# Performance work log

Measured on AMD Instinct MI355X. Metric: run time of the kernel, lower is better.

## Reference

```python
import jax, jax.numpy as jnp
import numpy as np

BN_EPS = 1e-3  # TF batch_norm default epsilon


def _three_nn(xyz1, xyz2):
    # xyz1: [B,N,3], xyz2: [B,M,3] -> squared dists [B,N,3], idx [B,N,3]
    d = (jnp.sum(xyz1 * xyz1, -1)[:, :, None]
         - 2.0 * jnp.einsum('bnd,bmd->bnm', xyz1, xyz2)
         + jnp.sum(xyz2 * xyz2, -1)[:, None, :])  # [B,N,M]
    neg, idx = jax.lax.top_k(-d, 3)
    return -neg, idx


def _conv_bn(x, W, b, g, beta, act):
    # 1x1 conv == dense over channel dim; BN over batch+point axes (B,N)
    y = jnp.einsum('bnc,cd->bnd', x, W) + b
    mu = jnp.mean(y, axis=(0, 1))
    var = jnp.var(y, axis=(0, 1))
    y = (y - mu) * jax.lax.rsqrt(var + BN_EPS) * g + beta
    return jax.nn.relu(y) if act else y


def setup_inputs() -> dict:
    key = jax.random.key(0)
    ks = jax.random.split(key, 6)
    B, N, M, C1, C2 = 16, 4096, 1024, 128, 256
    xyz1 = jax.random.normal(ks[0], (B, N, 3), jnp.float32)
    xyz2 = jax.random.normal(ks[1], (B, M, 3), jnp.float32)
    points1 = jax.random.normal(ks[2], (B, N, C1), jnp.float32)
    points2 = jax.random.normal(ks[3], (B, M, C2), jnp.float32)
    Cin = C1 + C2
    W0 = jax.random.normal(ks[4], (Cin, 256), jnp.float32) * (1.0 / np.sqrt(Cin))
    W1 = jax.random.normal(ks[5], (256, 128), jnp.float32) * (1.0 / np.sqrt(256))
    return {
        'xyz1': xyz1, 'points1': points1, 'xyz2': xyz2, 'points2': points2,
        'W0': W0, 'b0': jnp.zeros((256,), jnp.float32),
        'g0': jnp.ones((256,), jnp.float32), 'be0': jnp.zeros((256,), jnp.float32),
        'W1': W1, 'b1': jnp.zeros((128,), jnp.float32),
        'g1': jnp.ones((128,), jnp.float32), 'be1': jnp.zeros((128,), jnp.float32),
    }


def reference(xyz1, points1, xyz2, points2, W0, b0, g0, be0, W1, b1, g1, be1):
    dist, idx = _three_nn(xyz1, xyz2)            # [B,N,3]
    dist = jnp.maximum(dist, 1e-10)
    w = 1.0 / dist
    w = w / jnp.sum(w, axis=2, keepdims=True)    # [B,N,3]
    B = points2.shape[0]
    bidx = jnp.arange(B)[:, None, None]
    nbr = points2[bidx, idx]                     # [B,N,3,C2] gather
    interp = jnp.einsum('bnk,bnkc->bnc', w, nbr)
    x = jnp.concatenate([interp, points1], axis=2)  # [B,N,C1+C2]
    x = _conv_bn(x, W0, b0, g0, be0, act=True)
    x = _conv_bn(x, W1, b1, g1, be1, act=True)   # last_mlp_activation=True
    return x
```

## Files before the change

kernel.cpp:

```cpp
#include <hip/hip_runtime.h>
#include <hip/hip_bf16.h>
#include <stdint.h>

typedef __attribute__((ext_vector_type(4))) float f32x4;
typedef __attribute__((ext_vector_type(2))) float f32x2;
typedef __attribute__((ext_vector_type(8))) __bf16 bf16x8;

__device__ __forceinline__ unsigned short f2bf(float f) {
  unsigned u = __float_as_uint(f);
  unsigned r = (u + 0x7fffu + ((u >> 16) & 1u)) >> 16;
  return (unsigned short)r;
}
__device__ __forceinline__ float bf2f(unsigned short h) {
  return __uint_as_float(((unsigned)h) << 16);
}

__device__ __forceinline__ void load_lds16(const void* g, void* l) {
  __builtin_amdgcn_global_load_lds(
      (const __attribute__((address_space(1))) unsigned int*)g,
      (__attribute__((address_space(3))) unsigned int*)l, 16, 0, 0);
}

__device__ __forceinline__ void vwait(int n) {
  switch (n) {
    case 8: asm volatile("s_waitcnt vmcnt(8)" ::: "memory"); break;
    case 6: asm volatile("s_waitcnt vmcnt(6)" ::: "memory"); break;
    case 4: asm volatile("s_waitcnt vmcnt(4)" ::: "memory"); break;
    case 3: asm volatile("s_waitcnt vmcnt(3)" ::: "memory"); break;
    default: asm volatile("s_waitcnt vmcnt(0)" ::: "memory"); break;
  }
  __builtin_amdgcn_sched_barrier(0);
}

__global__ __launch_bounds__(256) void prep_kernel(
    const float* __restrict__ W0, const float* __restrict__ W1,
    const float* __restrict__ P2f, unsigned short* __restrict__ W0t,
    unsigned short* __restrict__ W1t, unsigned short* __restrict__ P2) {
  int id = blockIdx.x * 256 + threadIdx.x;
  if (id < 256 * 384) {
    int n = id / 384, k = id - n * 384;
    W0t[id] = f2bf(W0[k * 256 + n]);
  }
  if (id < 128 * 256) {
    int n = id / 256, k = id - n * 256;
    W1t[id] = f2bf(W1[k * 128 + n]);
  }
  if (id < 1048576) {
    f32x4 v = ((const f32x4*)P2f)[id];
    ushort4 o = make_ushort4(f2bf(v[0]), f2bf(v[1]), f2bf(v[2]), f2bf(v[3]));
    ((ushort4*)P2)[id] = o;
  }
}

__global__ __launch_bounds__(256) void three_nn_kernel(
    const float* __restrict__ xyz1, const float* __restrict__ xyz2,
    float* __restrict__ W3, int* __restrict__ I3) {
  __shared__ __align__(16) float sx[1024];
  __shared__ __align__(16) float sy[1024];
  __shared__ __align__(16) float sz[1024];
  __shared__ __align__(16) float sn[1024];
  const int b = blockIdx.y;
  const int n0 = blockIdx.x * 32;
  const int tid = threadIdx.x;

  const float* xb = xyz2 + (size_t)b * 3072;
  for (int i = tid; i < 1024; i += 256) {
    float x = xb[i * 3 + 0], y = xb[i * 3 + 1], z = xb[i * 3 + 2];
    sx[i] = x; sy[i] = y; sz[i] = z;
    sn[i] = x * x + y * y + z * z;
  }
  __syncthreads();

  const int pt = tid >> 3, q = tid & 7;
  const int n = n0 + pt;
  const float* p = xyz1 + ((size_t)b * 4096 + n) * 3;
  const float px = p[0], py = p[1], pz = p[2];
  const float cx = -2.f * px, cy = -2.f * py, cz = -2.f * pz;

  float d0 = 3e38f, d1 = 3e38f, d2 = 3e38f;
  int i0 = 0, i1 = 0, i2 = 0;
  auto ins = [&](float e, int j) {
    const bool c0 = e < d0, c1 = e < d1, c2 = e < d2;
    const float nd2 = c1 ? d1 : (c2 ? e : d2);
    const int   ni2 = c1 ? i1 : (c2 ? j : i2);
    const float nd1 = c0 ? d0 : (c1 ? e : d1);
    const int   ni1 = c0 ? i0 : (c1 ? j : i1);
    d0 = c0 ? e : d0; i0 = c0 ? j : i0;
    d1 = nd1; i1 = ni1;
    d2 = nd2; i2 = ni2;
  };

  const f32x4* vx = (const f32x4*)sx;
  const f32x4* vy = (const f32x4*)sy;
  const f32x4* vz = (const f32x4*)sz;
  const f32x4* vn = (const f32x4*)sn;
  for (int jj = 0; jj < 32; jj++) {
    const int c = jj * 8 + q;
    f32x4 ax = vx[c], ay = vy[c], az = vz[c], an = vn[c];
#pragma unroll
    for (int u = 0; u < 4; u++) {
      float d = fmaf(ax[u], cx, fmaf(ay[u], cy, fmaf(az[u], cz, an[u])));
      ins(d, c * 4 + u);
    }
  }
#pragma unroll
  for (int off = 1; off <= 4; off <<= 1) {
    float e0 = __shfl_xor(d0, off, 64);
    float e1 = __shfl_xor(d1, off, 64);
    float e2 = __shfl_xor(d2, off, 64);
    int j0 = __shfl_xor(i0, off, 64);
    int j1 = __shfl_xor(i1, off, 64);
    int j2 = __shfl_xor(i2, off, 64);
    ins(e0, j0); ins(e1, j1); ins(e2, j2);
  }

  if (q == 0) {
    const float pn = fmaf(px, px, fmaf(py, py, pz * pz));
    float t0 = fmaxf(d0 + pn, 1e-10f);
    float t1 = fmaxf(d1 + pn, 1e-10f);
    float t2 = fmaxf(d2 + pn, 1e-10f);
    float w0 = 1.f / t0, w1 = 1.f / t1, w2 = 1.f / t2;
    float inv = 1.f / (w0 + w1 + w2);
    const int row = b * 4096 + n;
    W3[row * 3 + 0] = w0 * inv;
    W3[row * 3 + 1] = w1 * inv;
    W3[row * 3 + 2] = w2 * inv;
    I3[row * 3 + 0] = (b << 10) + i0;
    I3[row * 3 + 1] = (b << 10) + i1;
    I3[row * 3 + 2] = (b << 10) + i2;
  }
}

__global__ __launch_bounds__(256) void interp_concat_kernel(
    const float* __restrict__ points1, const unsigned short* __restrict__ P2,
    const float* __restrict__ W3, const int* __restrict__ I3,
    unsigned short* __restrict__ X) {
  const int gw = blockIdx.x * 4 + (threadIdx.x >> 6);
  const int lane = threadIdx.x & 63;
#pragma unroll 2
  for (int pp = 0; pp < 8; pp++) {
    const int row = gw * 8 + pp;
    const float w0 = W3[row * 3 + 0], w1 = W3[row * 3 + 1], w2 = W3[row * 3 + 2];
    const int g0 = I3[row * 3 + 0], g1 = I3[row * 3 + 1], g2 = I3[row * 3 + 2];
    const ushort4 a0 = *(const ushort4*)(P2 + (size_t)g0 * 256 + lane * 4);
    const ushort4 a1 = *(const ushort4*)(P2 + (size_t)g1 * 256 + lane * 4);
    const ushort4 a2 = *(const ushort4*)(P2 + (size_t)g2 * 256 + lane * 4);
    float o0 = bf2f(a0.x) * w0 + bf2f(a1.x) * w1 + bf2f(a2.x) * w2;
    float o1 = bf2f(a0.y) * w0 + bf2f(a1.y) * w1 + bf2f(a2.y) * w2;
    float o2 = bf2f(a0.z) * w0 + bf2f(a1.z) * w1 + bf2f(a2.z) * w2;
    float o3 = bf2f(a0.w) * w0 + bf2f(a1.w) * w1 + bf2f(a2.w) * w2;
    unsigned int lo = (unsigned)f2bf(o0) | ((unsigned)f2bf(o1) << 16);
    unsigned int hi = (unsigned)f2bf(o2) | ((unsigned)f2bf(o3) << 16);
    *(uint2*)(X + (size_t)row * 384 + lane * 4) = make_uint2(lo, hi);
    const f32x2 qv = ((const f32x2*)(points1 + (size_t)row * 128))[lane];
    unsigned int pq = (unsigned)f2bf(qv.x) | ((unsigned)f2bf(qv.y) << 16);
    *(unsigned int*)(X + (size_t)row * 384 + 256 + lane * 2) = pq;
  }
}

__global__ __launch_bounds__(512) void gemm1_kernel(
    const unsigned short* __restrict__ A, const unsigned short* __restrict__ Bt,
    const float* __restrict__ bvec, unsigned short* __restrict__ Y,
    float* __restrict__ ssum, float* __restrict__ ssq) {
  __shared__ __align__(16) char smem[131072];
  unsigned short* S = (unsigned short*)smem;
  const int m0 = blockIdx.x * 256;
  const int tid = threadIdx.x;
  const int wv = tid >> 6, lane = tid & 63;
  const int wm = wv >> 2, wn = wv & 3;
  f32x4 acc[8][4] = {};

  auto stage = [&](int t) {
    const int k0 = t * 32;
    unsigned short* Ab = S + (t & 3) * 16384;
    unsigned short* Bb = Ab + 8192;
#pragma unroll
    for (int i = 0; i < 2; i++) {
      const int c = (wv * 2 + i) * 64 + lane;
      const int row = c >> 2, kp = c & 3;
      const int gk = (kp ^ (row & 3)) * 8;
      load_lds16(A + (size_t)(m0 + row) * 384 + k0 + gk, Ab + (wv * 2 + i) * 512);
      load_lds16(Bt + (size_t)row * 384 + k0 + gk, Bb + (wv * 2 + i) * 512);
    }
  };

  stage(0); stage(1); stage(2);
  for (int t = 0; t < 12; ++t) {
    const int w = 11 - t;
    vwait(w >= 2 ? 8 : w * 4);
    __builtin_amdgcn_s_barrier();
    __builtin_amdgcn_sched_barrier(0);
    if (t < 9) stage(t + 3);
    const unsigned short* Ab = S + (t & 3) * 16384;
    const unsigned short* Bb = Ab + 8192;
    const int q = lane >> 4;
    bf16x8 af[8], bfr[4];
#pragma unroll
    for (int mf = 0; mf < 8; mf++) {
      const int r = wm * 128 + mf * 16 + (lane & 15);
      af[mf] = *(const bf16x8*)(Ab + r * 32 + (q ^ (r & 3)) * 8);
    }
#pragma unroll
    for (int nf = 0; nf < 4; nf++) {
      const int c = wn * 64 + nf * 16 + (lane & 15);
      bfr[nf] = *(const bf16x8*)(Bb + c * 32 + (q ^ (c & 3)) * 8);
    }
    __builtin_amdgcn_s_setprio(1);
#pragma unroll
    for (int mf = 0; mf < 8; mf++)
#pragma unroll
      for (int nf = 0; nf < 4; nf++)
        acc[mf][nf] = __builtin_amdgcn_mfma_f32_16x16x32_bf16(
            af[mf], bfr[nf], acc[mf][nf], 0, 0, 0);
    __builtin_amdgcn_s_setprio(0);
  }
  __syncthreads();

  float s[4] = {0, 0, 0, 0}, s2[4] = {0, 0, 0, 0};
  unsigned short* ep = S + wv * 8192;
#pragma unroll
  for (int mf = 0; mf < 8; mf++) {
#pragma unroll
    for (int nf = 0; nf < 4; nf++) {
      const float bv = bvec[wn * 64 + nf * 16 + (lane & 15)];
      f32x4 v = acc[mf][nf];
#pragma unroll
      for (int r = 0; r < 4; r++) {
        float y = v[r] + bv;
        s[nf] += y;
        s2[nf] += y * y;
        ep[(mf * 16 + (lane >> 4) * 4 + r) * 64 + nf * 16 + (lane & 15)] =
            f2bf(y);
      }
    }
  }
#pragma unroll
  for (int it = 0; it < 16; it++) {
    const int rr = it * 8 + (lane >> 3);
    *(uint4*)(Y + (size_t)(m0 + wm * 128 + rr) * 256 + wn * 64 + (lane & 7) * 8) =
        *(const uint4*)(ep + rr * 64 + (lane & 7) * 8);
  }

#pragma unroll
  for (int nf = 0; nf < 4; nf++) {
    s[nf] += __shfl_xor(s[nf], 16, 64);
    s[nf] += __shfl_xor(s[nf], 32, 64);
    s2[nf] += __shfl_xor(s2[nf], 16, 64);
    s2[nf] += __shfl_xor(s2[nf], 32, 64);
  }
  if (lane < 16) {
#pragma unroll
    for (int nf = 0; nf < 4; nf++) {
      const int col = wn * 64 + nf * 16 + lane;
      atomicAdd(&ssum[col], s[nf]);
      atomicAdd(&ssq[col], s2[nf]);
    }
  }
}

__device__ __forceinline__ uint4 bnpack8(bf16x8 r, f32x4 s0, f32x4 s1,
                                         f32x4 c0, f32x4 c1) {
  unsigned short o[8];
#pragma unroll
  for (int j = 0; j < 8; j++) {
    const float sj = j < 4 ? s0[j] : s1[j - 4];
    const float cj = j < 4 ? c0[j] : c1[j - 4];
    o[j] = f2bf(fmaxf(0.f, fmaf((float)r[j], sj, cj)));
  }
  return make_uint4((unsigned)o[0] | ((unsigned)o[1] << 16),
                    (unsigned)o[2] | ((unsigned)o[3] << 16),
                    (unsigned)o[4] | ((unsigned)o[5] << 16),
                    (unsigned)o[6] | ((unsigned)o[7] << 16));
}

__global__ __launch_bounds__(512) void gemm2_kernel(
    const unsigned short* __restrict__ Yin, const unsigned short* __restrict__ Bt,
    const float* __restrict__ scale1, const float* __restrict__ bias1,
    const float* __restrict__ bvec, unsigned short* __restrict__ Y2,
    float* __restrict__ ssum, float* __restrict__ ssq) {
  __shared__ __align__(16) char smem[100352];
  unsigned short* S = (unsigned short*)smem;
  float* scL = (float*)(smem + 98304);
  float* biL = scL + 256;
  const int m0 = blockIdx.x * 256;
  const int tid = threadIdx.x;
  const int wv = tid >> 6, lane = tid & 63;
  const int wm = wv >> 2, wn = wv & 3;
  f32x4 acc[8][2] = {};

  if (tid < 256) scL[tid] = scale1[tid];
  else biL[tid - 256] = bias1[tid - 256];
  __syncthreads();

  bf16x8 arg[3][2];
  auto stageT = [&](int t, bf16x8(&ar)[2]) {
    const int k0 = t * 32;
#pragma unroll
    for (int j = 0; j < 2; j++) {
      const int c = tid + j * 512;
      const int row = c >> 2, kp = c & 3;
      const int gk = (kp ^ (row & 3)) * 8;
      ar[j] = *(const bf16x8*)(Yin + (size_t)(m0 + row) * 256 + k0 + gk);
    }
    const int cb = wv * 64 + lane;
    const int rowb = cb >> 2, kpb = cb & 3;
    const int gkb = (kpb ^ (rowb & 3)) * 8;
    load_lds16(Bt + (size_t)rowb * 256 + k0 + gkb,
               S + (t & 3) * 12288 + 8192 + wv * 512);
  };

  stageT(0, arg[0]); stageT(1, arg[1]); stageT(2, arg[2]);
#pragma unroll
  for (int t = 0; t < 8; ++t) {
    const int w = 7 - t;
    vwait(w >= 2 ? 6 : w * 3);
    unsigned short* Ab = S + (t & 3) * 12288;
#pragma unroll
    for (int j = 0; j < 2; j++) {
      const int c = tid + j * 512;
      const int row = c >> 2, kp = c & 3;
      const int gk = (kp ^ (row & 3)) * 8;
      const int kch = t * 32 + gk;
      const f32x4 sA = *(const f32x4*)(scL + kch);
      const f32x4 sB = *(const f32x4*)(scL + kch + 4);
      const f32x4 cA = *(const f32x4*)(biL + kch);
      const f32x4 cB = *(const f32x4*)(biL + kch + 4);
      *(uint4*)(Ab + c * 8) = bnpack8(arg[t % 3][j], sA, sB, cA, cB);
    }
    asm volatile("s_waitcnt lgkmcnt(0)" ::: "memory");
    __builtin_amdgcn_sched_barrier(0);
    __builtin_amdgcn_s_barrier();
    __builtin_amdgcn_sched_barrier(0);
    if (t < 5) stageT(t + 3, arg[t % 3]);
    const unsigned short* Bb = S + (t & 3) * 12288 + 8192;
    const int q = lane >> 4;
    bf16x8 af[8], bfr[2];
#pragma unroll
    for (int mf = 0; mf < 8; mf++) {
      const int r = wm * 128 + mf * 16 + (lane & 15);
      af[mf] = *(const bf16x8*)(Ab + r * 32 + (q ^ (r & 3)) * 8);
    }
#pragma unroll
    for (int nf = 0; nf < 2; nf++) {
      const int c = wn * 32 + nf * 16 + (lane & 15);
      bfr[nf] = *(const bf16x8*)(Bb + c * 32 + (q ^ (c & 3)) * 8);
    }
    __builtin_amdgcn_s_setprio(1);
#pragma unroll
    for (int mf = 0; mf < 8; mf++)
#pragma unroll
      for (int nf = 0; nf < 2; nf++)
        acc[mf][nf] = __builtin_amdgcn_mfma_f32_16x16x32_bf16(
            af[mf], bfr[nf], acc[mf][nf], 0, 0, 0);
    __builtin_amdgcn_s_setprio(0);
  }
  __syncthreads();

  float s[2] = {0, 0}, s2[2] = {0, 0};
  unsigned short* ep = S + wv * 4096;
#pragma unroll
  for (int mf = 0; mf < 8; mf++) {
#pragma unroll
    for (int nf = 0; nf < 2; nf++) {
      const float bv = bvec[wn * 32 + nf * 16 + (lane & 15)];
      f32x4 v = acc[mf][nf];
#pragma unroll
      for (int r = 0; r < 4; r++) {
        float y = v[r] + bv;
        s[nf] += y;
        s2[nf] += y * y;
        ep[(mf * 16 + (lane >> 4) * 4 + r) * 32 + nf * 16 + (lane & 15)] =
            f2bf(y);
      }
    }
  }
#pragma unroll
  for (int it = 0; it < 8; it++) {
    const int rr = it * 16 + (lane >> 2);
    *(uint4*)(Y2 + (size_t)(m0 + wm * 128 + rr) * 128 + wn * 32 + (lane & 3) * 8) =
        *(const uint4*)(ep + rr * 32 + (lane & 3) * 8);
  }

#pragma unroll
  for (int nf = 0; nf < 2; nf++) {
    s[nf] += __shfl_xor(s[nf], 16, 64);
    s[nf] += __shfl_xor(s[nf], 32, 64);
    s2[nf] += __shfl_xor(s2[nf], 16, 64);
    s2[nf] += __shfl_xor(s2[nf], 32, 64);
  }
  if (lane < 16) {
#pragma unroll
    for (int nf = 0; nf < 2; nf++) {
      const int col = wn * 32 + nf * 16 + lane;
      atomicAdd(&ssum[col], s[nf]);
      atomicAdd(&ssq[col], s2[nf]);
    }
  }
}

__global__ void bn_fin_kernel(const float* __restrict__ ssum,
                              const float* __restrict__ ssq,
                              const float* __restrict__ g,
                              const float* __restrict__ be,
                              float* __restrict__ scale,
                              float* __restrict__ bias, int C) {
  int c = blockIdx.x * blockDim.x + threadIdx.x;
  if (c < C) {
    const float invN = 1.0f / 65536.0f;
    float mu = ssum[c] * invN;
    float var = ssq[c] * invN - mu * mu;
    float sc = g[c] * rsqrtf(var + 1e-3f);
    scale[c] = sc;
    bias[c] = be[c] - mu * sc;
  }
}

__global__ __launch_bounds__(256) void bnrelu_out_kernel(
    const unsigned short* __restrict__ Y2, const float* __restrict__ scale,
    const float* __restrict__ bias, float* __restrict__ out) {
  const size_t i = ((size_t)blockIdx.x * 256 + threadIdx.x) * 8;
  const int c0 = (int)(i & 127);
  uint4 v = *(const uint4*)(Y2 + i);
  const f32x4 sA = *(const f32x4*)(scale + c0);
  const f32x4 sB = *(const f32x4*)(scale + c0 + 4);
  const f32x4 bA = *(const f32x4*)(bias + c0);
  const f32x4 bB = *(const f32x4*)(bias + c0 + 4);
  unsigned int w[4] = {v.x, v.y, v.z, v.w};
  f32x4 o0, o1;
#pragma unroll
  for (int q = 0; q < 2; q++) {
    o0[q * 2 + 0] = fmaxf(0.f, fmaf(bf2f((unsigned short)(w[q] & 0xffff)), sA[q * 2 + 0], bA[q * 2 + 0]));
    o0[q * 2 + 1] = fmaxf(0.f, fmaf(bf2f((unsigned short)(w[q] >> 16)),   sA[q * 2 + 1], bA[q * 2 + 1]));
    o1[q * 2 + 0] = fmaxf(0.f, fmaf(bf2f((unsigned short)(w[q + 2] & 0xffff)), sB[q * 2 + 0], bB[q * 2 + 0]));
    o1[q * 2 + 1] = fmaxf(0.f, fmaf(bf2f((unsigned short)(w[q + 2] >> 16)),   sB[q * 2 + 1], bB[q * 2 + 1]));
  }
  *(f32x4*)(out + i) = o0;
  *(f32x4*)(out + i + 4) = o1;
}

extern "C" void kernel_launch(void* const* d_in, const int* in_sizes, int n_in,
                              void* d_out, int out_size, void* d_ws,
                              size_t ws_size, hipStream_t stream) {
  const float* xyz1 = (const float*)d_in[0];
  const float* points1 = (const float*)d_in[1];
  const float* xyz2 = (const float*)d_in[2];
  const float* points2 = (const float*)d_in[3];
  const float* W0 = (const float*)d_in[4];
  const float* b0 = (const float*)d_in[5];
  const float* g0 = (const float*)d_in[6];
  const float* be0 = (const float*)d_in[7];
  const float* W1 = (const float*)d_in[8];
  const float* b1 = (const float*)d_in[9];
  const float* g1 = (const float*)d_in[10];
  const float* be1 = (const float*)d_in[11];

  char* ws = (char*)d_ws;
  unsigned short* X = (unsigned short*)(ws);
  unsigned short* Y2 = (unsigned short*)(ws);
  unsigned short* Y = (unsigned short*)(ws + 50331648);
  unsigned short* P2 = (unsigned short*)(ws + 50331648);
  float* W3 = (float*)(ws + 50331648 + 8388608);
  int* I3 = (int*)(ws + 50331648 + 8388608 + 786432);
  unsigned short* W0t = (unsigned short*)(ws + 83886080);
  unsigned short* W1t = (unsigned short*)(ws + 84082688);
  float* stats = (float*)(ws + 84148224);
  float* sum1 = stats, *sq1 = stats + 256, *scale1 = stats + 512, *bias1 = stats + 768;
  float* sum2 = stats + 1024, *sq2 = stats + 1152, *scale2 = stats + 1280, *bias2 = stats + 1408;
  float* outF = (float*)d_out;

  hipMemsetAsync(stats, 0, 1536 * sizeof(float), stream);
  prep_kernel<<<4096, 256, 0, stream>>>(W0, W1, points2, W0t, W1t, P2);
  three_nn_kernel<<<dim3(128, 16), 256, 0, stream>>>(xyz1, xyz2, W3, I3);
  interp_concat_kernel<<<2048, 256, 0, stream>>>(points1, P2, W3, I3, X);
  gemm1_kernel<<<256, 512, 0, stream>>>(X, W0t, b0, Y, sum1, sq1);
  bn_fin_kernel<<<1, 256, 0, stream>>>(sum1, sq1, g0, be0, scale1, bias1, 256);
  gemm2_kernel<<<256, 512, 0, stream>>>(Y, W1t, scale1, bias1, b1, Y2, sum2, sq2);
  bn_fin_kernel<<<1, 128, 0, stream>>>(sum2, sq2, g1, be1, scale2, bias2, 128);
  bnrelu_out_kernel<<<4096, 256, 0, stream>>>(Y2, scale2, bias2, outF);
}
```

Before: 139.2 us.

## Fuse BatchNorm finalize and apply into GEMMs via cooperative grid sync

Both GEMM kernels now keep their accumulators in registers, atomically reduce the per-channel statistics, grid-synchronize, compute the BN scale and bias locally, then apply BN+ReLU before writing. Y now holds the post-ReLU activations and gemm2 writes the final fp32 output directly. This removes the two bn_fin launches, the separate bnrelu_out pass, the bf16 Y2 round trip and the on-the-fly BN in gemm2's A-staging, which now uses plain direct-to-LDS loads. In exchange it depends on cooperative launch with all 256 blocks co-resident and adds a grid-wide barrier stall per GEMM.

```diff
diff --git a/kernel.cpp b/kernel.cpp
--- a/kernel.cpp
+++ b/kernel.cpp
@@ -1,6 +1,9 @@
 #include <hip/hip_runtime.h>
 #include <hip/hip_bf16.h>
+#include <hip/hip_cooperative_groups.h>
 #include <stdint.h>
+
+namespace cg = cooperative_groups;
 
 typedef __attribute__((ext_vector_type(4))) float f32x4;
 typedef __attribute__((ext_vector_type(2))) float f32x2;
@@ -160,7 +163,8 @@
 
 __global__ __launch_bounds__(512) void gemm1_kernel(
     const unsigned short* __restrict__ A, const unsigned short* __restrict__ Bt,
-    const float* __restrict__ bvec, unsigned short* __restrict__ Y,
+    const float* __restrict__ bvec, const float* __restrict__ g0,
+    const float* __restrict__ be0, unsigned short* __restrict__ Y,
     float* __restrict__ ssum, float* __restrict__ ssq) {
   __shared__ __align__(16) char smem[131072];
   unsigned short* S = (unsigned short*)smem;
@@ -214,33 +218,22 @@
             af[mf], bfr[nf], acc[mf][nf], 0, 0, 0);
     __builtin_amdgcn_s_setprio(0);
   }
-  __syncthreads();
-
-  float s[4] = {0, 0, 0, 0}, s2[4] = {0, 0, 0, 0};
-  unsigned short* ep = S + wv * 8192;
-#pragma unroll
-  for (int mf = 0; mf < 8; mf++) {
+
+  float bvl[4], s[4] = {0, 0, 0, 0}, s2[4] = {0, 0, 0, 0};
+#pragma unroll
+  for (int nf = 0; nf < 4; nf++) bvl[nf] = bvec[wn * 64 + nf * 16 + (lane & 15)];
+#pragma unroll
+  for (int mf = 0; mf < 8; mf++)
 #pragma unroll
     for (int nf = 0; nf < 4; nf++) {
-      const float bv = bvec[wn * 64 + nf * 16 + (lane & 15)];
       f32x4 v = acc[mf][nf];
 #pragma unroll
       for (int r = 0; r < 4; r++) {
-        float y = v[r] + bv;
+        float y = v[r] + bvl[nf];
         s[nf] += y;
         s2[nf] += y * y;
-        ep[(mf * 16 + (lane >> 4) * 4 + r) * 64 + nf * 16 + (lane & 15)] =
-            f2bf(y);
       }
     }
-  }
-#pragma unroll
-  for (int it = 0; it < 16; it++) {
-    const int rr = it * 8 + (lane >> 3);
-    *(uint4*)(Y + (size_t)(m0 + wm * 128 + rr) * 256 + wn * 64 + (lane & 7) * 8) =
-        *(const uint4*)(ep + rr * 64 + (lane & 7) * 8);
-  }
-
 #pragma unroll
   for (int nf = 0; nf < 4; nf++) {
     s[nf] += __shfl_xor(s[nf], 16, 64);
@@ -256,83 +249,82 @@
       atomicAdd(&ssq[col], s2[nf]);
     }
   }
-}
-
-__device__ __forceinline__ uint4 bnpack8(bf16x8 r, f32x4 s0, f32x4 s1,
-                                         f32x4 c0, f32x4 c1) {
-  unsigned short o[8];
-#pragma unroll
-  for (int j = 0; j < 8; j++) {
-    const float sj = j < 4 ? s0[j] : s1[j - 4];
-    const float cj = j < 4 ? c0[j] : c1[j - 4];
-    o[j] = f2bf(fmaxf(0.f, fmaf((float)r[j], sj, cj)));
-  }
-  return make_uint4((unsigned)o[0] | ((unsigned)o[1] << 16),
-                    (unsigned)o[2] | ((unsigned)o[3] << 16),
-                    (unsigned)o[4] | ((unsigned)o[5] << 16),
-                    (unsigned)o[6] | ((unsigned)o[7] << 16));
+
+  cg::this_grid().sync();
+
+  const float invN = 1.0f / 65536.0f;
+  float scl[4], bil[4];
+#pragma unroll
+  for (int nf = 0; nf < 4; nf++) {
+    const int col = wn * 64 + nf * 16 + (lane & 15);
+    float mu = ssum[col] * invN;
+    float var = ssq[col] * invN - mu * mu;
+    float sc = g0[col] * rsqrtf(var + 1e-3f);
+    scl[nf] = sc;
+    bil[nf] = be0[col] - mu * sc;
+  }
+
+  unsigned short* ep = S + wv * 8192;
+#pragma unroll
+  for (int mf = 0; mf < 8; mf++) {
+#pragma unroll
+    for (int nf = 0; nf < 4; nf++) {
+      f32x4 v = acc[mf][nf];
+#pragma unroll
+      for (int r = 0; r < 4; r++) {
+        float y = fmaxf(0.f, fmaf(v[r] + bvl[nf], scl[nf], bil[nf]));
+        ep[(mf * 16 + (lane >> 4) * 4 + r) * 64 + nf * 16 + (lane & 15)] =
+            f2bf(y);
+      }
+    }
+  }
+#pragma unroll
+  for (int it = 0; it < 16; it++) {
+    const int rr = it * 8 + (lane >> 3);
+    *(uint4*)(Y + (size_t)(m0 + wm * 128 + rr) * 256 + wn * 64 + (lane & 7) * 8) =
+        *(const uint4*)(ep + rr * 64 + (lane & 7) * 8);
+  }
 }
 
 __global__ __launch_bounds__(512) void gemm2_kernel(
     const unsigned short* __restrict__ Yin, const unsigned short* __restrict__ Bt,
-    const float* __restrict__ scale1, const float* __restrict__ bias1,
-    const float* __restrict__ bvec, unsigned short* __restrict__ Y2,
+    const float* __restrict__ bvec, const float* __restrict__ g1,
+    const float* __restrict__ be1, float* __restrict__ out,
     float* __restrict__ ssum, float* __restrict__ ssq) {
-  __shared__ __align__(16) char smem[100352];
+  __shared__ __align__(16) char smem[98304];
   unsigned short* S = (unsigned short*)smem;
-  float* scL = (float*)(smem + 98304);
-  float* biL = scL + 256;
   const int m0 = blockIdx.x * 256;
   const int tid = threadIdx.x;
   const int wv = tid >> 6, lane = tid & 63;
   const int wm = wv >> 2, wn = wv & 3;
   f32x4 acc[8][2] = {};
 
-  if (tid < 256) scL[tid] = scale1[tid];
-  else biL[tid - 256] = bias1[tid - 256];
-  __syncthreads();
-
-  bf16x8 arg[3][2];
-  auto stageT = [&](int t, bf16x8(&ar)[2]) {
+  auto stage = [&](int t) {
     const int k0 = t * 32;
+    unsigned short* Ab = S + (t & 3) * 12288;
+    unsigned short* Bb = Ab + 8192;
 #pragma unroll
     for (int j = 0; j < 2; j++) {
       const int c = tid + j * 512;
       const int row = c >> 2, kp = c & 3;
       const int gk = (kp ^ (row & 3)) * 8;
-      ar[j] = *(const bf16x8*)(Yin + (size_t)(m0 + row) * 256 + k0 + gk);
-    }
-    const int cb = wv * 64 + lane;
+      load_lds16(Yin + (size_t)(m0 + row) * 256 + k0 + gk, Ab + c * 8);
+    }
+    const int cb = tid;
     const int rowb = cb >> 2, kpb = cb & 3;
     const int gkb = (kpb ^ (rowb & 3)) * 8;
-    load_lds16(Bt + (size_t)rowb * 256 + k0 + gkb,
-               S + (t & 3) * 12288 + 8192 + wv * 512);
+    load_lds16(Bt + (size_t)rowb * 256 + k0 + gkb, Bb + cb * 8);
   };
 
-  stageT(0, arg[0]); stageT(1, arg[1]); stageT(2, arg[2]);
-#pragma unroll
+  stage(0); stage(1); stage(2);
   for (int t = 0; t < 8; ++t) {
     const int w = 7 - t;
     vwait(w >= 2 ? 6 : w * 3);
-    unsigned short* Ab = S + (t & 3) * 12288;
-#pragma unroll
-    for (int j = 0; j < 2; j++) {
-      const int c = tid + j * 512;
-      const int row = c >> 2, kp = c & 3;
-      const int gk = (kp ^ (row & 3)) * 8;
-      const int kch = t * 32 + gk;
-      const f32x4 sA = *(const f32x4*)(scL + kch);
-      const f32x4 sB = *(const f32x4*)(scL + kch + 4);
-      const f32x4 cA = *(const f32x4*)(biL + kch);
-      const f32x4 cB = *(const f32x4*)(biL + kch + 4);
-      *(uint4*)(Ab + c * 8) = bnpack8(arg[t % 3][j], sA, sB, cA, cB);
-    }
-    asm volatile("s_waitcnt lgkmcnt(0)" ::: "memory");
-    __builtin_amdgcn_sched_barrier(0);
     __builtin_amdgcn_s_barrier();
     __builtin_amdgcn_sched_barrier(0);
-    if (t < 5) stageT(t + 3, arg[t % 3]);
-    const unsigned short* Bb = S + (t & 3) * 12288 + 8192;
+    if (t < 5) stage(t + 3);
+    const unsigned short* Ab = S + (t & 3) * 12288;
+    const unsigned short* Bb = Ab + 8192;
     const int q = lane >> 4;
     bf16x8 af[8], bfr[2];
 #pragma unroll
@@ -354,33 +346,22 @@
             af[mf], bfr[nf], acc[mf][nf], 0, 0, 0);
     __builtin_amdgcn_s_setprio(0);
   }
-  __syncthreads();
-
-  float s[2] = {0, 0}, s2[2] = {0, 0};
-  unsigned short* ep = S + wv * 4096;
-#pragma unroll
-  for (int mf = 0; mf < 8; mf++) {
+
+  float bvl[2], s[2] = {0, 0}, s2[2] = {0, 0};
+#pragma unroll
+  for (int nf = 0; nf < 2; nf++) bvl[nf] = bvec[wn * 32 + nf * 16 + (lane & 15)];
+#pragma unroll
+  for (int mf = 0; mf < 8; mf++)
 #pragma unroll
     for (int nf = 0; nf < 2; nf++) {
-      const float bv = bvec[wn * 32 + nf * 16 + (lane & 15)];
       f32x4 v = acc[mf][nf];
 #pragma unroll
       for (int r = 0; r < 4; r++) {
-        float y = v[r] + bv;
+        float y = v[r] + bvl[nf];
         s[nf] += y;
         s2[nf] += y * y;
-        ep[(mf * 16 + (lane >> 4) * 4 + r) * 32 + nf * 16 + (lane & 15)] =
-            f2bf(y);
       }
     }
-  }
-#pragma unroll
-  for (int it = 0; it < 8; it++) {
-    const int rr = it * 16 + (lane >> 2);
-    *(uint4*)(Y2 + (size_t)(m0 + wm * 128 + rr) * 128 + wn * 32 + (lane & 3) * 8) =
-        *(const uint4*)(ep + rr * 32 + (lane & 3) * 8);
-  }
-
 #pragma unroll
   for (int nf = 0; nf < 2; nf++) {
     s[nf] += __shfl_xor(s[nf], 16, 64);
@@ -396,46 +377,44 @@
       atomicAdd(&ssq[col], s2[nf]);
     }
   }
-}
-
-__global__ void bn_fin_kernel(const float* __restrict__ ssum,
-                              const float* __restrict__ ssq,
-                              const float* __restrict__ g,
-                              const float* __restrict__ be,
-                              float* __restrict__ scale,
-                              float* __restrict__ bias, int C) {
-  int c = blockIdx.x * blockDim.x + threadIdx.x;
-  if (c < C) {
-    const float invN = 1.0f / 65536.0f;
-    float mu = ssum[c] * invN;
-    float var = ssq[c] * invN - mu * mu;
-    float sc = g[c] * rsqrtf(var + 1e-3f);
-    scale[c] = sc;
-    bias[c] = be[c] - mu * sc;
-  }
-}
-
-__global__ __launch_bounds__(256) void bnrelu_out_kernel(
-    const unsigned short* __restrict__ Y2, const float* __restrict__ scale,
-    const float* __restrict__ bias, float* __restrict__ out) {
-  const size_t i = ((size_t)blockIdx.x * 256 + threadIdx.x) * 8;
-  const int c0 = (int)(i & 127);
-  uint4 v = *(const uint4*)(Y2 + i);
-  const f32x4 sA = *(const f32x4*)(scale + c0);
-  const f32x4 sB = *(const f32x4*)(scale + c0 + 4);
-  const f32x4 bA = *(const f32x4*)(bias + c0);
-  const f32x4 bB = *(const f32x4*)(bias + c0 + 4);
-  unsigned int w[4] = {v.x, v.y, v.z, v.w};
-  f32x4 o0, o1;
-#pragma unroll
-  for (int q = 0; q < 2; q++) {
-    o0[q * 2 + 0] = fmaxf(0.f, fmaf(bf2f((unsigned short)(w[q] & 0xffff)), sA[q * 2 + 0], bA[q * 2 + 0]));
-    o0[q * 2 + 1] = fmaxf(0.f, fmaf(bf2f((unsigned short)(w[q] >> 16)),   sA[q * 2 + 1], bA[q * 2 + 1]));
-    o1[q * 2 + 0] = fmaxf(0.f, fmaf(bf2f((unsigned short)(w[q + 2] & 0xffff)), sB[q * 2 + 0], bB[q * 2 + 0]));
-    o1[q * 2 + 1] = fmaxf(0.f, fmaf(bf2f((unsigned short)(w[q + 2] >> 16)),   sB[q * 2 + 1], bB[q * 2 + 1]));
-  }
-  *(f32x4*)(out + i) = o0;
-  *(f32x4*)(out + i + 4) = o1;
+
+  cg::this_grid().sync();
+
+  const float invN = 1.0f / 65536.0f;
+  float scl[2], bil[2];
+#pragma unroll
+  for (int nf = 0; nf < 2; nf++) {
+    const int col = wn * 32 + nf * 16 + (lane & 15);
+    float mu = ssum[col] * invN;
+    float var = ssq[col] * invN - mu * mu;
+    float sc = g1[col] * rsqrtf(var + 1e-3f);
+    scl[nf] = sc;
+    bil[nf] = be1[col] - mu * sc;
+  }
+
+  float* ep = (float*)smem + wv * 2048;
+#pragma unroll
+  for (int h = 0; h < 2; h++) {
+#pragma unroll
+    for (int mh = 0; mh < 4; mh++) {
+      const int mf = h * 4 + mh;
+#pragma unroll
+      for (int nf = 0; nf < 2; nf++) {
+        f32x4 v = acc[mf][nf];
+#pragma unroll
+        for (int r = 0; r < 4; r++) {
+          float y = fmaxf(0.f, fmaf(v[r] + bvl[nf], scl[nf], bil[nf]));
+          ep[(mh * 16 + (lane >> 4) * 4 + r) * 32 + nf * 16 + (lane & 15)] = y;
+        }
+      }
+    }
+#pragma unroll
+    for (int it = 0; it < 8; it++) {
+      const int rr = it * 8 + (lane >> 3);
+      *(f32x4*)(out + (size_t)(m0 + wm * 128 + h * 64 + rr) * 128 + wn * 32 +
+                (lane & 7) * 4) = *(const f32x4*)(ep + rr * 32 + (lane & 7) * 4);
+    }
+  }
 }
 
 extern "C" void kernel_launch(void* const* d_in, const int* in_sizes, int n_in,
@@ -456,7 +435,6 @@
 
   char* ws = (char*)d_ws;
   unsigned short* X = (unsigned short*)(ws);
-  unsigned short* Y2 = (unsigned short*)(ws);
   unsigned short* Y = (unsigned short*)(ws + 50331648);
   unsigned short* P2 = (unsigned short*)(ws + 50331648);
   float* W3 = (float*)(ws + 50331648 + 8388608);
@@ -464,17 +442,27 @@
   unsigned short* W0t = (unsigned short*)(ws + 83886080);
   unsigned short* W1t = (unsigned short*)(ws + 84082688);
   float* stats = (float*)(ws + 84148224);
-  float* sum1 = stats, *sq1 = stats + 256, *scale1 = stats + 512, *bias1 = stats + 768;
-  float* sum2 = stats + 1024, *sq2 = stats + 1152, *scale2 = stats + 1280, *bias2 = stats + 1408;
+  float* sum1 = stats;
+  float* sq1 = stats + 256;
+  float* sum2 = stats + 512;
+  float* sq2 = stats + 640;
   float* outF = (float*)d_out;
 
-  hipMemsetAsync(stats, 0, 1536 * sizeof(float), stream);
+  hipMemsetAsync(stats, 0, 768 * sizeof(float), stream);
   prep_kernel<<<4096, 256, 0, stream>>>(W0, W1, points2, W0t, W1t, P2);
   three_nn_kernel<<<dim3(128, 16), 256, 0, stream>>>(xyz1, xyz2, W3, I3);
   interp_concat_kernel<<<2048, 256, 0, stream>>>(points1, P2, W3, I3, X);
-  gemm1_kernel<<<256, 512, 0, stream>>>(X, W0t, b0, Y, sum1, sq1);
-  bn_fin_kernel<<<1, 256, 0, stream>>>(sum1, sq1, g0, be0, scale1, bias1, 256);
-  gemm2_kernel<<<256, 512, 0, stream>>>(Y, W1t, scale1, bias1, b1, Y2, sum2, sq2);
-  bn_fin_kernel<<<1, 128, 0, stream>>>(sum2, sq2, g1, be1, scale2, bias2, 128);
-  bnrelu_out_kernel<<<4096, 256, 0, stream>>>(Y2, scale2, bias2, outF);
-}
+
+  {
+    void* args[] = {(void*)&X, (void*)&W0t, (void*)&b0, (void*)&g0,
+                    (void*)&be0, (void*)&Y, (void*)&sum1, (void*)&sq1};
+    hipLaunchCooperativeKernel((void*)gemm1_kernel, dim3(256), dim3(512), args,
+                               0, stream);
+  }
+  {
+    void* args[] = {(void*)&Y, (void*)&W1t, (void*)&b1, (void*)&g1,
+                    (void*)&be1, (void*)&outF, (void*)&sum2, (void*)&sq2};
+    hipLaunchCooperativeKernel((void*)gemm2_kernel, dim3(256), dim3(512), args,
+                               0, stream);
+  }
+}
```

Measured after the change: 193.9 us. 39.3% more time.

## Halve GEMM row tiles to 128 and shrink pipeline depth for occupancy

Applied to the files above, without the earlier changes.

Both GEMM kernels now process 128 rows per block instead of 256, which doubles the grid to 512 blocks so all CUs on the MI355X receive work. The LDS pipeline drops from 4 to 3 buffers with a prefetch distance of 2 instead of 3, and the vmcnt waits are adjusted to match. LDS use and accumulator registers shrink, and a launch_bounds hint asks for more resident blocks. The trade-off is more reloading of the weight operand across blocks and less latency hiding per block.

```diff
diff --git a/kernel.cpp b/kernel.cpp
--- a/kernel.cpp
+++ b/kernel.cpp
@@ -23,10 +23,9 @@
 
 __device__ __forceinline__ void vwait(int n) {
   switch (n) {
-    case 8: asm volatile("s_waitcnt vmcnt(8)" ::: "memory"); break;
-    case 6: asm volatile("s_waitcnt vmcnt(6)" ::: "memory"); break;
     case 4: asm volatile("s_waitcnt vmcnt(4)" ::: "memory"); break;
     case 3: asm volatile("s_waitcnt vmcnt(3)" ::: "memory"); break;
+    case 2: asm volatile("s_waitcnt vmcnt(2)" ::: "memory"); break;
     default: asm volatile("s_waitcnt vmcnt(0)" ::: "memory"); break;
   }
   __builtin_amdgcn_sched_barrier(0);
@@ -158,46 +157,51 @@
   }
 }
 
-__global__ __launch_bounds__(512) void gemm1_kernel(
+__global__ __launch_bounds__(512, 4) void gemm1_kernel(
     const unsigned short* __restrict__ A, const unsigned short* __restrict__ Bt,
     const float* __restrict__ bvec, unsigned short* __restrict__ Y,
     float* __restrict__ ssum, float* __restrict__ ssq) {
-  __shared__ __align__(16) char smem[131072];
+  __shared__ __align__(16) char smem[73728];
   unsigned short* S = (unsigned short*)smem;
-  const int m0 = blockIdx.x * 256;
+  const int m0 = blockIdx.x * 128;
   const int tid = threadIdx.x;
   const int wv = tid >> 6, lane = tid & 63;
   const int wm = wv >> 2, wn = wv & 3;
-  f32x4 acc[8][4] = {};
+  f32x4 acc[4][4] = {};
 
   auto stage = [&](int t) {
     const int k0 = t * 32;
-    unsigned short* Ab = S + (t & 3) * 16384;
-    unsigned short* Bb = Ab + 8192;
-#pragma unroll
-    for (int i = 0; i < 2; i++) {
-      const int c = (wv * 2 + i) * 64 + lane;
+    unsigned short* Ab = S + (t % 3) * 12288;
+    unsigned short* Bb = Ab + 4096;
+    {
+      const int c = tid;
       const int row = c >> 2, kp = c & 3;
       const int gk = (kp ^ (row & 3)) * 8;
-      load_lds16(A + (size_t)(m0 + row) * 384 + k0 + gk, Ab + (wv * 2 + i) * 512);
-      load_lds16(Bt + (size_t)row * 384 + k0 + gk, Bb + (wv * 2 + i) * 512);
+      load_lds16(A + (size_t)(m0 + row) * 384 + k0 + gk, Ab + c * 8);
+    }
+#pragma unroll
+    for (int j = 0; j < 2; j++) {
+      const int c = tid + j * 512;
+      const int row = c >> 2, kp = c & 3;
+      const int gk = (kp ^ (row & 3)) * 8;
+      load_lds16(Bt + (size_t)row * 384 + k0 + gk, Bb + c * 8);
     }
   };
 
-  stage(0); stage(1); stage(2);
+  stage(0); stage(1);
+#pragma unroll
   for (int t = 0; t < 12; ++t) {
-    const int w = 11 - t;
-    vwait(w >= 2 ? 8 : w * 4);
+    vwait(t < 11 ? 3 : 0);
     __builtin_amdgcn_s_barrier();
     __builtin_amdgcn_sched_barrier(0);
-    if (t < 9) stage(t + 3);
-    const unsigned short* Ab = S + (t & 3) * 16384;
-    const unsigned short* Bb = Ab + 8192;
+    if (t < 10) stage(t + 2);
+    const unsigned short* Ab = S + (t % 3) * 12288;
+    const unsigned short* Bb = Ab + 4096;
     const int q = lane >> 4;
-    bf16x8 af[8], bfr[4];
-#pragma unroll
-    for (int mf = 0; mf < 8; mf++) {
-      const int r = wm * 128 + mf * 16 + (lane & 15);
+    bf16x8 af[4], bfr[4];
+#pragma unroll
+    for (int mf = 0; mf < 4; mf++) {
+      const int r = wm * 64 + mf * 16 + (lane & 15);
       af[mf] = *(const bf16x8*)(Ab + r * 32 + (q ^ (r & 3)) * 8);
     }
 #pragma unroll
@@ -207,7 +211,7 @@
     }
     __builtin_amdgcn_s_setprio(1);
 #pragma unroll
-    for (int mf = 0; mf < 8; mf++)
+    for (int mf = 0; mf < 4; mf++)
 #pragma unroll
       for (int nf = 0; nf < 4; nf++)
         acc[mf][nf] = __builtin_amdgcn_mfma_f32_16x16x32_bf16(
@@ -216,17 +220,18 @@
   }
   __syncthreads();
 
-  float s[4] = {0, 0, 0, 0}, s2[4] = {0, 0, 0, 0};
-  unsigned short* ep = S + wv * 8192;
-#pragma unroll
-  for (int mf = 0; mf < 8; mf++) {
+  float bvl[4], s[4] = {0, 0, 0, 0}, s2[4] = {0, 0, 0, 0};
+#pragma unroll
+  for (int nf = 0; nf < 4; nf++) bvl[nf] = bvec[wn * 64 + nf * 16 + (lane & 15)];
+  unsigned short* ep = S + wv * 4096;
+#pragma unroll
+  for (int mf = 0; mf < 4; mf++) {
 #pragma unroll
     for (int nf = 0; nf < 4; nf++) {
-      const float bv = bvec[wn * 64 + nf * 16 + (lane & 15)];
       f32x4 v = acc[mf][nf];
 #pragma unroll
       for (int r = 0; r < 4; r++) {
-        float y = v[r] + bv;
+        float y = v[r] + bvl[nf];
         s[nf] += y;
         s2[nf] += y * y;
         ep[(mf * 16 + (lane >> 4) * 4 + r) * 64 + nf * 16 + (lane & 15)] =
@@ -235,9 +240,9 @@
     }
   }
 #pragma unroll
-  for (int it = 0; it < 16; it++) {
+  for (int it = 0; it < 8; it++) {
     const int rr = it * 8 + (lane >> 3);
-    *(uint4*)(Y + (size_t)(m0 + wm * 128 + rr) * 256 + wn * 64 + (lane & 7) * 8) =
+    *(uint4*)(Y + (size_t)(m0 + wm * 64 + rr) * 256 + wn * 64 + (lane & 7) * 8) =
         *(const uint4*)(ep + rr * 64 + (lane & 7) * 8);
   }
 
@@ -273,81 +278,70 @@
                     (unsigned)o[6] | ((unsigned)o[7] << 16));
 }
 
-__global__ __launch_bounds__(512) void gemm2_kernel(
+__global__ __launch_bounds__(512, 4) void gemm2_kernel(
     const unsigned short* __restrict__ Yin, const unsigned short* __restrict__ Bt,
     const float* __restrict__ scale1, const float* __restrict__ bias1,
     const float* __restrict__ bvec, unsigned short* __restrict__ Y2,
     float* __restrict__ ssum, float* __restrict__ ssq) {
-  __shared__ __align__(16) char smem[100352];
+  __shared__ __align__(16) char smem[43008];
   unsigned short* S = (unsigned short*)smem;
-  float* scL = (float*)(smem + 98304);
+  unsigned short* Bs = S + 8192;
+  float* scL = (float*)(smem + 40960);
   float* biL = scL + 256;
-  const int m0 = blockIdx.x * 256;
+  const int m0 = blockIdx.x * 128;
   const int tid = threadIdx.x;
   const int wv = tid >> 6, lane = tid & 63;
   const int wm = wv >> 2, wn = wv & 3;
-  f32x4 acc[8][2] = {};
+  f32x4 acc[4][2] = {};
 
   if (tid < 256) scL[tid] = scale1[tid];
   else biL[tid - 256] = bias1[tid - 256];
   __syncthreads();
 
-  bf16x8 arg[3][2];
-  auto stageT = [&](int t, bf16x8(&ar)[2]) {
+  const int c = tid, arow = c >> 2, kp = c & 3;
+  const int gk = (kp ^ (arow & 3)) * 8;
+
+  bf16x8 arg[2];
+  auto stageT = [&](int t, bf16x8& ar) {
     const int k0 = t * 32;
-#pragma unroll
-    for (int j = 0; j < 2; j++) {
-      const int c = tid + j * 512;
-      const int row = c >> 2, kp = c & 3;
-      const int gk = (kp ^ (row & 3)) * 8;
-      ar[j] = *(const bf16x8*)(Yin + (size_t)(m0 + row) * 256 + k0 + gk);
-    }
-    const int cb = wv * 64 + lane;
-    const int rowb = cb >> 2, kpb = cb & 3;
-    const int gkb = (kpb ^ (rowb & 3)) * 8;
-    load_lds16(Bt + (size_t)rowb * 256 + k0 + gkb,
-               S + (t & 3) * 12288 + 8192 + wv * 512);
+    ar = *(const bf16x8*)(Yin + (size_t)(m0 + arow) * 256 + k0 + gk);
+    load_lds16(Bt + (size_t)arow * 256 + k0 + gk, Bs + (t % 3) * 4096 + c * 8);
   };
 
-  stageT(0, arg[0]); stageT(1, arg[1]); stageT(2, arg[2]);
+  stageT(0, arg[0]); stageT(1, arg[1]);
 #pragma unroll
   for (int t = 0; t < 8; ++t) {
-    const int w = 7 - t;
-    vwait(w >= 2 ? 6 : w * 3);
-    unsigned short* Ab = S + (t & 3) * 12288;
-#pragma unroll
-    for (int j = 0; j < 2; j++) {
-      const int c = tid + j * 512;
-      const int row = c >> 2, kp = c & 3;
-      const int gk = (kp ^ (row & 3)) * 8;
+    vwait(t < 7 ? 2 : 0);
+    unsigned short* Ab = S + (t & 1) * 4096;
+    {
       const int kch = t * 32 + gk;
       const f32x4 sA = *(const f32x4*)(scL + kch);
       const f32x4 sB = *(const f32x4*)(scL + kch + 4);
       const f32x4 cA = *(const f32x4*)(biL + kch);
       const f32x4 cB = *(const f32x4*)(biL + kch + 4);
-      *(uint4*)(Ab + c * 8) = bnpack8(arg[t % 3][j], sA, sB, cA, cB);
+      *(uint4*)(Ab + c * 8) = bnpack8(arg[t & 1], sA, sB, cA, cB);
     }
     asm volatile("s_waitcnt lgkmcnt(0)" ::: "memory");
     __builtin_amdgcn_sched_barrier(0);
     __builtin_amdgcn_s_barrier();
     __builtin_amdgcn_sched_barrier(0);
-    if (t < 5) stageT(t + 3, arg[t % 3]);
-    const unsigned short* Bb = S + (t & 3) * 12288 + 8192;
+    if (t < 6) stageT(t + 2, arg[t & 1]);
+    const unsigned short* Bb = Bs + (t % 3) * 4096;
     const int q = lane >> 4;
-    bf16x8 af[8], bfr[2];
-#pragma unroll
-    for (int mf = 0; mf < 8; mf++) {
-      const int r = wm * 128 + mf * 16 + (lane & 15);
+    bf16x8 af[4], bfr[2];
+#pragma unroll
+    for (int mf = 0; mf < 4; mf++) {
+      const int r = wm * 64 + mf * 16 + (lane & 15);
       af[mf] = *(const bf16x8*)(Ab + r * 32 + (q ^ (r & 3)) * 8);
     }
 #pragma unroll
     for (int nf = 0; nf < 2; nf++) {
-      const int c = wn * 32 + nf * 16 + (lane & 15);
-      bfr[nf] = *(const bf16x8*)(Bb + c * 32 + (q ^ (c & 3)) * 8);
+      const int cc = wn * 32 + nf * 16 + (lane & 15);
+      bfr[nf] = *(const bf16x8*)(Bb + cc * 32 + (q ^ (cc & 3)) * 8);
     }
     __builtin_amdgcn_s_setprio(1);
 #pragma unroll
-    for (int mf = 0; mf < 8; mf++)
+    for (int mf = 0; mf < 4; mf++)
 #pragma unroll
       for (int nf = 0; nf < 2; nf++)
         acc[mf][nf] = __builtin_amdgcn_mfma_f32_16x16x32_bf16(
@@ -356,17 +350,18 @@
   }
   __syncthreads();
 
-  float s[2] = {0, 0}, s2[2] = {0, 0};
-  unsigned short* ep = S + wv * 4096;
-#pragma unroll
-  for (int mf = 0; mf < 8; mf++) {
+  float bvl[2], s[2] = {0, 0}, s2[2] = {0, 0};
+#pragma unroll
+  for (int nf = 0; nf < 2; nf++) bvl[nf] = bvec[wn * 32 + nf * 16 + (lane & 15)];
+  unsigned short* ep = S + wv * 2048;
+#pragma unroll
+  for (int mf = 0; mf < 4; mf++) {
 #pragma unroll
     for (int nf = 0; nf < 2; nf++) {
-      const float bv = bvec[wn * 32 + nf * 16 + (lane & 15)];
       f32x4 v = acc[mf][nf];
 #pragma unroll
       for (int r = 0; r < 4; r++) {
-        float y = v[r] + bv;
+        float y = v[r] + bvl[nf];
         s[nf] += y;
         s2[nf] += y * y;
         ep[(mf * 16 + (lane >> 4) * 4 + r) * 32 + nf * 16 + (lane & 15)] =
@@ -375,9 +370,9 @@
     }
   }
 #pragma unroll
-  for (int it = 0; it < 8; it++) {
+  for (int it = 0; it < 4; it++) {
     const int rr = it * 16 + (lane >> 2);
-    *(uint4*)(Y2 + (size_t)(m0 + wm * 128 + rr) * 128 + wn * 32 + (lane & 3) * 8) =
+    *(uint4*)(Y2 + (size_t)(m0 + wm * 64 + rr) * 128 + wn * 32 + (lane & 3) * 8) =
         *(const uint4*)(ep + rr * 32 + (lane & 3) * 8);
   }
 
@@ -472,9 +467,9 @@
   prep_kernel<<<4096, 256, 0, stream>>>(W0, W1, points2, W0t, W1t, P2);
   three_nn_kernel<<<dim3(128, 16), 256, 0, stream>>>(xyz1, xyz2, W3, I3);
   interp_concat_kernel<<<2048, 256, 0, stream>>>(points1, P2, W3, I3, X);
-  gemm1_kernel<<<256, 512, 0, stream>>>(X, W0t, b0, Y, sum1, sq1);
+  gemm1_kernel<<<512, 512, 0, stream>>>(X, W0t, b0, Y, sum1, sq1);
   bn_fin_kernel<<<1, 256, 0, stream>>>(sum1, sq1, g0, be0, scale1, bias1, 256);
-  gemm2_kernel<<<256, 512, 0, stream>>>(Y, W1t, scale1, bias1, b1, Y2, sum2, sq2);
+  gemm2_kernel<<<512, 512, 0, stream>>>(Y, W1t, scale1, bias1, b1, Y2, sum2, sq2);
   bn_fin_kernel<<<1, 128, 0, stream>>>(sum2, sq2, g1, be1, scale2, bias2, 128);
   bnrelu_out_kernel<<<4096, 256, 0, stream>>>(Y2, scale2, bias2, outF);
 }
```

Measured after the change: 155.6 us. 11.8% more time.

## Fuse weight prep, three-NN search and interpolation into one kernel

Applied to the files above, without the earlier changes.

Merges the prep, three-NN and interpolate/concat kernels into a single launch. Each block finds the neighbours for its 32 points, keeps the weights and indices in shared memory, then gathers fp32 points2 rows directly instead of reading a separately converted bf16 copy. Two extra blocks handle the weight transposes. This removes two launches, the W3/I3 round trip through global memory and the points2 bf16 conversion pass, but the gather now reads fp32 rows, which doubles the bytes fetched per neighbour.

```diff
diff --git a/kernel.cpp b/kernel.cpp
--- a/kernel.cpp
+++ b/kernel.cpp
@@ -32,36 +32,38 @@
   __builtin_amdgcn_sched_barrier(0);
 }
 
-__global__ __launch_bounds__(256) void prep_kernel(
+__global__ __launch_bounds__(256) void nn_fused_kernel(
+    const float* __restrict__ xyz1, const float* __restrict__ xyz2,
+    const float* __restrict__ points1, const float* __restrict__ points2,
     const float* __restrict__ W0, const float* __restrict__ W1,
-    const float* __restrict__ P2f, unsigned short* __restrict__ W0t,
-    unsigned short* __restrict__ W1t, unsigned short* __restrict__ P2) {
-  int id = blockIdx.x * 256 + threadIdx.x;
-  if (id < 256 * 384) {
-    int n = id / 384, k = id - n * 384;
-    W0t[id] = f2bf(W0[k * 256 + n]);
-  }
-  if (id < 128 * 256) {
-    int n = id / 256, k = id - n * 256;
-    W1t[id] = f2bf(W1[k * 128 + n]);
-  }
-  if (id < 1048576) {
-    f32x4 v = ((const f32x4*)P2f)[id];
-    ushort4 o = make_ushort4(f2bf(v[0]), f2bf(v[1]), f2bf(v[2]), f2bf(v[3]));
-    ((ushort4*)P2)[id] = o;
-  }
-}
-
-__global__ __launch_bounds__(256) void three_nn_kernel(
-    const float* __restrict__ xyz1, const float* __restrict__ xyz2,
-    float* __restrict__ W3, int* __restrict__ I3) {
+    unsigned short* __restrict__ W0t, unsigned short* __restrict__ W1t,
+    unsigned short* __restrict__ X) {
+  const int bid = blockIdx.x;
+  const int tid = threadIdx.x;
+  if (bid >= 2048) {
+    if (bid == 2048) {
+      for (int id = tid; id < 98304; id += 256) {
+        int n = id / 384, k = id - n * 384;
+        W0t[id] = f2bf(W0[k * 256 + n]);
+      }
+    } else {
+      for (int id = tid; id < 32768; id += 256) {
+        int n = id / 256, k = id - n * 256;
+        W1t[id] = f2bf(W1[k * 128 + n]);
+      }
+    }
+    return;
+  }
+
   __shared__ __align__(16) float sx[1024];
   __shared__ __align__(16) float sy[1024];
   __shared__ __align__(16) float sz[1024];
   __shared__ __align__(16) float sn[1024];
-  const int b = blockIdx.y;
-  const int n0 = blockIdx.x * 32;
-  const int tid = threadIdx.x;
+  __shared__ float sw[32][3];
+  __shared__ int si[32][3];
+
+  const int b = bid >> 7;
+  const int n0 = (bid & 127) * 32;
 
   const float* xb = xyz2 + (size_t)b * 3072;
   for (int i = tid; i < 1024; i += 256) {
@@ -71,84 +73,78 @@
   }
   __syncthreads();
 
-  const int pt = tid >> 3, q = tid & 7;
-  const int n = n0 + pt;
-  const float* p = xyz1 + ((size_t)b * 4096 + n) * 3;
-  const float px = p[0], py = p[1], pz = p[2];
-  const float cx = -2.f * px, cy = -2.f * py, cz = -2.f * pz;
-
-  float d0 = 3e38f, d1 = 3e38f, d2 = 3e38f;
-  int i0 = 0, i1 = 0, i2 = 0;
-  auto ins = [&](float e, int j) {
-    const bool c0 = e < d0, c1 = e < d1, c2 = e < d2;
-    const float nd2 = c1 ? d1 : (c2 ? e : d2);
-    const int   ni2 = c1 ? i1 : (c2 ? j : i2);
-    const float nd1 = c0 ? d0 : (c1 ? e : d1);
-    const int   ni1 = c0 ? i0 : (c1 ? j : i1);
-    d0 = c0 ? e : d0; i0 = c0 ? j : i0;
-    d1 = nd1; i1 = ni1;
-    d2 = nd2; i2 = ni2;
-  };
-
-  const f32x4* vx = (const f32x4*)sx;
-  const f32x4* vy = (const f32x4*)sy;
-  const f32x4* vz = (const f32x4*)sz;
-  const f32x4* vn = (const f32x4*)sn;
-  for (int jj = 0; jj < 32; jj++) {
-    const int c = jj * 8 + q;
-    f32x4 ax = vx[c], ay = vy[c], az = vz[c], an = vn[c];
-#pragma unroll
-    for (int u = 0; u < 4; u++) {
-      float d = fmaf(ax[u], cx, fmaf(ay[u], cy, fmaf(az[u], cz, an[u])));
-      ins(d, c * 4 + u);
-    }
-  }
-#pragma unroll
-  for (int off = 1; off <= 4; off <<= 1) {
-    float e0 = __shfl_xor(d0, off, 64);
-    float e1 = __shfl_xor(d1, off, 64);
-    float e2 = __shfl_xor(d2, off, 64);
-    int j0 = __shfl_xor(i0, off, 64);
-    int j1 = __shfl_xor(i1, off, 64);
-    int j2 = __shfl_xor(i2, off, 64);
-    ins(e0, j0); ins(e1, j1); ins(e2, j2);
-  }
-
-  if (q == 0) {
-    const float pn = fmaf(px, px, fmaf(py, py, pz * pz));
-    float t0 = fmaxf(d0 + pn, 1e-10f);
-    float t1 = fmaxf(d1 + pn, 1e-10f);
-    float t2 = fmaxf(d2 + pn, 1e-10f);
-    float w0 = 1.f / t0, w1 = 1.f / t1, w2 = 1.f / t2;
-    float inv = 1.f / (w0 + w1 + w2);
-    const int row = b * 4096 + n;
-    W3[row * 3 + 0] = w0 * inv;
-    W3[row * 3 + 1] = w1 * inv;
-    W3[row * 3 + 2] = w2 * inv;
-    I3[row * 3 + 0] = (b << 10) + i0;
-    I3[row * 3 + 1] = (b << 10) + i1;
-    I3[row * 3 + 2] = (b << 10) + i2;
-  }
-}
-
-__global__ __launch_bounds__(256) void interp_concat_kernel(
-    const float* __restrict__ points1, const unsigned short* __restrict__ P2,
-    const float* __restrict__ W3, const int* __restrict__ I3,
-    unsigned short* __restrict__ X) {
-  const int gw = blockIdx.x * 4 + (threadIdx.x >> 6);
-  const int lane = threadIdx.x & 63;
+  {
+    const int pt = tid >> 3, q = tid & 7;
+    const int n = n0 + pt;
+    const float* p = xyz1 + ((size_t)b * 4096 + n) * 3;
+    const float px = p[0], py = p[1], pz = p[2];
+    const float cx = -2.f * px, cy = -2.f * py, cz = -2.f * pz;
+
+    float d0 = 3e38f, d1 = 3e38f, d2 = 3e38f;
+    int i0 = 0, i1 = 0, i2 = 0;
+    auto ins = [&](float e, int j) {
+      const bool c0 = e < d0, c1 = e < d1, c2 = e < d2;
+      const float nd2 = c1 ? d1 : (c2 ? e : d2);
+      const int   ni2 = c1 ? i1 : (c2 ? j : i2);
+      const float nd1 = c0 ? d0 : (c1 ? e : d1);
+      const int   ni1 = c0 ? i0 : (c1 ? j : i1);
+      d0 = c0 ? e : d0; i0 = c0 ? j : i0;
+      d1 = nd1; i1 = ni1;
+      d2 = nd2; i2 = ni2;
+    };
+
+    const f32x4* vx = (const f32x4*)sx;
+    const f32x4* vy = (const f32x4*)sy;
+    const f32x4* vz = (const f32x4*)sz;
+    const f32x4* vn = (const f32x4*)sn;
+    for (int jj = 0; jj < 32; jj++) {
+      const int c = jj * 8 + q;
+      f32x4 ax = vx[c], ay = vy[c], az = vz[c], an = vn[c];
+#pragma unroll
+      for (int u = 0; u < 4; u++) {
+        float d = fmaf(ax[u], cx, fmaf(ay[u], cy, fmaf(az[u], cz, an[u])));
+        ins(d, c * 4 + u);
+      }
+    }
+#pragma unroll
+    for (int off = 1; off <= 4; off <<= 1) {
+      float e0 = __shfl_xor(d0, off, 64);
+      float e1 = __shfl_xor(d1, off, 64);
+      float e2 = __shfl_xor(d2, off, 64);
+      int j0 = __shfl_xor(i0, off, 64);
+      int j1 = __shfl_xor(i1, off, 64);
+      int j2 = __shfl_xor(i2, off, 64);
+      ins(e0, j0); ins(e1, j1); ins(e2, j2);
+    }
+
+    if (q == 0) {
+      const float pn = fmaf(px, px, fmaf(py, py, pz * pz));
+      float t0 = fmaxf(d0 + pn, 1e-10f);
+      float t1 = fmaxf(d1 + pn, 1e-10f);
+      float t2 = fmaxf(d2 + pn, 1e-10f);
+      float w0 = 1.f / t0, w1 = 1.f / t1, w2 = 1.f / t2;
+      float inv = 1.f / (w0 + w1 + w2);
+      sw[pt][0] = w0 * inv; sw[pt][1] = w1 * inv; sw[pt][2] = w2 * inv;
+      si[pt][0] = (b << 10) + i0;
+      si[pt][1] = (b << 10) + i1;
+      si[pt][2] = (b << 10) + i2;
+    }
+  }
+  __syncthreads();
+
+  const int wv = tid >> 6, lane = tid & 63;
 #pragma unroll 2
   for (int pp = 0; pp < 8; pp++) {
-    const int row = gw * 8 + pp;
-    const float w0 = W3[row * 3 + 0], w1 = W3[row * 3 + 1], w2 = W3[row * 3 + 2];
-    const int g0 = I3[row * 3 + 0], g1 = I3[row * 3 + 1], g2 = I3[row * 3 + 2];
-    const ushort4 a0 = *(const ushort4*)(P2 + (size_t)g0 * 256 + lane * 4);
-    const ushort4 a1 = *(const ushort4*)(P2 + (size_t)g1 * 256 + lane * 4);
-    const ushort4 a2 = *(const ushort4*)(P2 + (size_t)g2 * 256 + lane * 4);
-    float o0 = bf2f(a0.x) * w0 + bf2f(a1.x) * w1 + bf2f(a2.x) * w2;
-    float o1 = bf2f(a0.y) * w0 + bf2f(a1.y) * w1 + bf2f(a2.y) * w2;
-    float o2 = bf2f(a0.z) * w0 + bf2f(a1.z) * w1 + bf2f(a2.z) * w2;
-    float o3 = bf2f(a0.w) * w0 + bf2f(a1.w) * w1 + bf2f(a2.w) * w2;
+    const int lr = wv * 8 + pp;
+    const int row = b * 4096 + n0 + lr;
+    const float w0 = sw[lr][0], w1 = sw[lr][1], w2 = sw[lr][2];
+    const f32x4 a0 = ((const f32x4*)(points2 + (size_t)si[lr][0] * 256))[lane];
+    const f32x4 a1 = ((const f32x4*)(points2 + (size_t)si[lr][1] * 256))[lane];
+    const f32x4 a2 = ((const f32x4*)(points2 + (size_t)si[lr][2] * 256))[lane];
+    float o0 = a0[0] * w0 + a1[0] * w1 + a2[0] * w2;
+    float o1 = a0[1] * w0 + a1[1] * w1 + a2[1] * w2;
+    float o2 = a0[2] * w0 + a1[2] * w1 + a2[2] * w2;
+    float o3 = a0[3] * w0 + a1[3] * w1 + a2[3] * w2;
     unsigned int lo = (unsigned)f2bf(o0) | ((unsigned)f2bf(o1) << 16);
     unsigned int hi = (unsigned)f2bf(o2) | ((unsigned)f2bf(o3) << 16);
     *(uint2*)(X + (size_t)row * 384 + lane * 4) = make_uint2(lo, hi);
@@ -458,9 +454,6 @@
   unsigned short* X = (unsigned short*)(ws);
   unsigned short* Y2 = (unsigned short*)(ws);
   unsigned short* Y = (unsigned short*)(ws + 50331648);
-  unsigned short* P2 = (unsigned short*)(ws + 50331648);
-  float* W3 = (float*)(ws + 50331648 + 8388608);
-  int* I3 = (int*)(ws + 50331648 + 8388608 + 786432);
   unsigned short* W0t = (unsigned short*)(ws + 83886080);
   unsigned short* W1t = (unsigned short*)(ws + 84082688);
   float* stats = (float*)(ws + 84148224);
@@ -469,9 +462,8 @@
   float* outF = (float*)d_out;
 
   hipMemsetAsync(stats, 0, 1536 * sizeof(float), stream);
-  prep_kernel<<<4096, 256, 0, stream>>>(W0, W1, points2, W0t, W1t, P2);
-  three_nn_kernel<<<dim3(128, 16), 256, 0, stream>>>(xyz1, xyz2, W3, I3);
-  interp_concat_kernel<<<2048, 256, 0, stream>>>(points1, P2, W3, I3, X);
+  nn_fused_kernel<<<2050, 256, 0, stream>>>(xyz1, xyz2, points1, points2, W0,
+                                            W1, W0t, W1t, X);
   gemm1_kernel<<<256, 512, 0, stream>>>(X, W0t, b0, Y, sum1, sq1);
   bn_fin_kernel<<<1, 256, 0, stream>>>(sum1, sq1, g0, be0, scale1, bias1, 256);
   gemm2_kernel<<<256, 512, 0, stream>>>(Y, W1t, scale1, bias1, b1, Y2, sum2, sq2);
```

New measurement: 167.3 us. 20.2% more time.
